# Kernel tuning notes

Measured on AMD Instinct MI355X. Metric: run time of the kernel, lower is better.

The kernel has to match this reference:

```python
import jax, jax.numpy as jnp
import numpy as np

CUBE_SIZE = 24
N_NEURONS = CUBE_SIZE ** 3  # 13824
INPUT_DIM = 512
OUTPUT_DIM = 1000
MAX_STEPS = 30
BATCH = 256


def _build_neighbor_indices(size: int) -> np.ndarray:
    """[N, 27] int32; invalid (out-of-cube) neighbors map to pad slot N."""
    n = size ** 3
    c = np.arange(size)
    z, y, x = np.meshgrid(c, c, c, indexing='ij')  # each [size,size,size]
    cols = []
    for dz in (-1, 0, 1):
        for dy in (-1, 0, 1):
            for dx in (-1, 0, 1):
                nz, ny, nx = z + dz, y + dy, x + dx
                valid = ((nz >= 0) & (nz < size) & (ny >= 0) & (ny < size)
                         & (nx >= 0) & (nx < size))
                idx = nz * size * size + ny * size + nx
                cols.append(np.where(valid, idx, n))
    return np.stack(cols, axis=-1).reshape(n, 27).astype(np.int32)


def setup_inputs() -> dict:
    key = jax.random.key(0)
    ks = jax.random.split(key, 4)
    # xavier-ish small init scales (gain 0.5 style)
    w_in = jax.random.normal(ks[0], (N_NEURONS, INPUT_DIM), jnp.float32) * 0.01
    w_local = jax.random.normal(ks[1], (N_NEURONS, 27), jnp.float32) * 0.1
    w_out = jax.random.normal(ks[2], (OUTPUT_DIM, N_NEURONS), jnp.float32) * 0.01
    x = jax.random.normal(ks[3], (BATCH, INPUT_DIM), jnp.float32)
    return {
        'x': x,
        'W_in_w': w_in,
        'W_in_b': jnp.zeros((N_NEURONS,), jnp.float32),
        'W_local': w_local,
        'W_out_w': w_out,
        'W_out_b': jnp.zeros((OUTPUT_DIM,), jnp.float32),
        'neighbor_indices': jnp.asarray(_build_neighbor_indices(CUBE_SIZE)),
    }


def reference(x, W_in_w, W_in_b, W_local, W_out_w, W_out_b, neighbor_indices):
    batch = x.shape[0]
    x_proj = x @ W_in_w.T + W_in_b  # [B, N]
    h0 = jnp.zeros((batch, N_NEURONS), x.dtype)
    pad = jnp.zeros((batch, 1), x.dtype)

    def step(h, _):
        h_padded = jnp.concatenate([h, pad], axis=1)        # [B, N+1]
        nbr = h_padded[:, neighbor_indices]                  # [B, N, 27]
        weighted = jnp.einsum('bnk,nk->bn', nbr, W_local)    # [B, N]
        return jnp.tanh(x_proj + weighted), None

    h, _ = jax.lax.scan(step, h0, None, length=MAX_STEPS)
    return h @ W_out_w.T + W_out_b  # [B, output_dim]
```

## Files before the change

kernel.cpp:

```cpp
#include <hip/hip_runtime.h>
#include <hip/hip_bf16.h>

#define NN   13824
#define BB   256
#define KDIM 512
#define ODIM 1000
#define CUBE 24
#define KS   16

typedef short bf8 __attribute__((ext_vector_type(8)));
typedef float f32x4 __attribute__((ext_vector_type(4)));

__device__ __forceinline__ float fast_tanh(float a) {
    float e = __expf(2.0f * a);
    return 1.0f - 2.0f / (e + 1.0f);
}
__device__ __forceinline__ float bf_lo(unsigned u) { return __uint_as_float(u << 16); }
__device__ __forceinline__ float bf_hi(unsigned u) { return __uint_as_float(u & 0xffff0000u); }
__device__ __forceinline__ unsigned short bf_rne(float f) {
    unsigned u = __float_as_uint(f);
    u += 0x7fffu + ((u >> 16) & 1u);
    return (unsigned short)(u >> 16);
}
__device__ __forceinline__ unsigned pk_bf16(float lo, float hi) {
    union { __hip_bfloat162 h; unsigned u; } cv;
    cv.h = __float22bfloat162_rn(make_float2(lo, hi));
    return cv.u;
}
__device__ __forceinline__ bf8 cvt8(float4 a, float4 b) {
    union { bf8 v; unsigned u[4]; } r;
    r.u[0] = pk_bf16(a.x, a.y);
    r.u[1] = pk_bf16(a.z, a.w);
    r.u[2] = pk_bf16(b.x, b.y);
    r.u[3] = pk_bf16(b.z, b.w);
    return r.v;
}

__global__ __launch_bounds__(256) void xbf_kernel(
    const float* __restrict__ x, unsigned* __restrict__ xb)
{
    int i = blockIdx.x * 256 + threadIdx.x;
    float2 v = *(const float2*)&x[(size_t)i * 2];
    xb[i] = pk_bf16(v.x, v.y);
}

__global__ __launch_bounds__(256) void xproj_mfma(
    const float* __restrict__ w_in, const float* __restrict__ bias,
    const short* __restrict__ xbf, unsigned short* __restrict__ xp,
    unsigned short* __restrict__ h1)
{
    const int tid = threadIdx.x, w = tid >> 6, lane = tid & 63;
    const int quad = lane >> 4, l16 = lane & 15;
    const int n0 = blockIdx.x * 16;
    const float* __restrict__ arow = &w_in[(size_t)(n0 + l16) * KDIM];

    f32x4 acc[4] = {};

    int ka = quad * 8;
    float4 a0 = *(const float4*)&arow[ka];
    float4 a1 = *(const float4*)&arow[ka + 4];
    bf8 bb[4];
#pragma unroll
    for (int j = 0; j < 4; ++j)
        bb[j] = *(const bf8*)&xbf[(size_t)(w * 64 + j * 16 + l16) * KDIM + ka];

    for (int it = 0; it < 16; ++it) {
        float4 na0{}, na1{}; bf8 nb[4] = {};
        if (it < 15) {
            const int nka = ka + 32;
            na0 = *(const float4*)&arow[nka];
            na1 = *(const float4*)&arow[nka + 4];
#pragma unroll
            for (int j = 0; j < 4; ++j)
                nb[j] = *(const bf8*)&xbf[(size_t)(w * 64 + j * 16 + l16) * KDIM + nka];
        }
        bf8 af = cvt8(a0, a1);
#pragma unroll
        for (int j = 0; j < 4; ++j)
            acc[j] = __builtin_amdgcn_mfma_f32_16x16x32_bf16(af, bb[j], acc[j], 0, 0, 0);
        a0 = na0; a1 = na1;
#pragma unroll
        for (int j = 0; j < 4; ++j) bb[j] = nb[j];
        ka += 32;
    }

#pragma unroll
    for (int j = 0; j < 4; ++j) {
        const int b = w * 64 + j * 16 + l16;
#pragma unroll
        for (int r = 0; r < 4; ++r) {
            const int n = n0 + quad * 4 + r;
            const float v = acc[j][r] + bias[n];
            xp[(size_t)n * BB + b] = bf_rne(v);
            h1[(size_t)n * BB + b] = bf_rne(fast_tanh(v));
        }
    }
}

__device__ __forceinline__ void load_plane_f2(
    const unsigned* __restrict__ h32, int z, int y, int xx, int dof, float2* w9)
{
#pragma unroll
    for (int j = 0; j < 9; ++j) {
        const int dz = j / 3 - 1, dy = j % 3 - 1;
        const int zz = z + dz, yy = y + dy;
        const bool valid = (xx >= 0) & (xx < CUBE) & (zz >= 0) & (zz < CUBE) &
                           (yy >= 0) & (yy < CUBE);
        unsigned v = 0u;
        if (valid) v = h32[(size_t)((zz * 24 + yy) * 24 + xx) * 128 + dof];
        w9[j] = make_float2(bf_lo(v), bf_hi(v));
    }
}

__global__ __launch_bounds__(256) void step_kernel(
    const unsigned* __restrict__ hprev, const unsigned* __restrict__ xp,
    const float* __restrict__ wl, unsigned* __restrict__ hnext)
{
    const int tid  = threadIdx.x;
    const int wid  = __builtin_amdgcn_readfirstlane(tid >> 6);
    const int wvb  = wid & 1;
    const int yoff = wid >> 1;
    const int lane = tid & 63;

    const int bid   = blockIdx.x;
    const int zhi   = bid & 7;
    const int inner = bid >> 3;
    const int yp    = inner % 12;
    const int r     = inner / 12;
    const int xc    = r & 3;
    const int zlo   = r >> 2;
    const int z     = zhi * 3 + zlo;
    const int y     = yp * 2 + yoff;

    const int x0   = xc * 6;
    const int dof  = wvb * 64 + lane;

    float2 win[5][9];
    load_plane_f2(hprev, z, y, x0 - 1, dof, win[0]);
    load_plane_f2(hprev, z, y, x0,     dof, win[1]);
    load_plane_f2(hprev, z, y, x0 + 1, dof, win[2]);
    load_plane_f2(hprev, z, y, x0 + 2, dof, win[3]);

#pragma unroll
    for (int xi = 0; xi < 6; ++xi) {
        const int x = x0 + xi;
        if (xi <= 3)
            load_plane_f2(hprev, z, y, x + 3, dof, win[(xi + 4) % 5]);

        const int n = (z * 24 + y) * 24 + x;
        const float* __restrict__ wn = &wl[(size_t)n * 27];
        const unsigned xpv = xp[(size_t)n * 128 + dof];
        float2 acc = make_float2(bf_lo(xpv), bf_hi(xpv));

        const float2* pm = win[xi % 5];
        const float2* pc = win[(xi + 1) % 5];
        const float2* pp = win[(xi + 2) % 5];
#pragma unroll
        for (int j = 0; j < 9; ++j) {
            const float w0 = wn[3 * j + 0];
            const float w1 = wn[3 * j + 1];
            const float w2 = wn[3 * j + 2];
            acc.x += w0 * pm[j].x + w1 * pc[j].x + w2 * pp[j].x;
            acc.y += w0 * pm[j].y + w1 * pc[j].y + w2 * pp[j].y;
        }
        hnext[(size_t)n * 128 + dof] = pk_bf16(fast_tanh(acc.x), fast_tanh(acc.y));
    }
}

__global__ __launch_bounds__(256) void transpose_kernel(
    const unsigned* __restrict__ h32, unsigned* __restrict__ hT32)
{
    __shared__ unsigned short T[64][66];
    const int tid = threadIdx.x;
    const int rr = tid >> 2, g = tid & 3;
    const int k0 = blockIdx.x * 64, b0 = blockIdx.y * 64;
#pragma unroll
    for (int i = 0; i < 8; ++i) {
        unsigned d = h32[(size_t)(k0 + rr) * 128 + b0 / 2 + g * 8 + i];
        const int bl = (g * 8 + i) * 2;
        T[bl][rr]     = (unsigned short)(d & 0xffffu);
        T[bl + 1][rr] = (unsigned short)(d >> 16);
    }
    __syncthreads();
#pragma unroll
    for (int i = 0; i < 8; ++i) {
        const int kl = (g * 8 + i) * 2;
        unsigned d = (unsigned)T[rr][kl] | ((unsigned)T[rr][kl + 1] << 16);
        hT32[(size_t)(b0 + rr) * (NN / 2) + k0 / 2 + g * 8 + i] = d;
    }
}

__global__ __launch_bounds__(256) void outgemm_mfma(
    const float* __restrict__ wout, const short* __restrict__ hT,
    float* __restrict__ part)
{
    const int tid = threadIdx.x, w = tid >> 6, lane = tid & 63;
    const int quad = lane >> 4, l16 = lane & 15;
    const int o0 = blockIdx.x * 128 + w * 32;
    const int kb = blockIdx.z * (NN / KS);
    const int b0 = blockIdx.y * 64;

    const int oa = o0 + l16, ob = o0 + 16 + l16;
    const bool av0 = oa < ODIM, av1 = ob < ODIM;
    const float* __restrict__ ar0 = &wout[(size_t)oa * NN];
    const float* __restrict__ ar1 = &wout[(size_t)ob * NN];
    const float4 z4 = {0.f, 0.f, 0.f, 0.f};

    f32x4 acc[2][4] = {};

    int ka = kb + quad * 8;
    float4 a00 = av0 ? *(const float4*)&ar0[ka]     : z4;
    float4 a01 = av0 ? *(const float4*)&ar0[ka + 4] : z4;
    float4 a10 = av1 ? *(const float4*)&ar1[ka]     : z4;
    float4 a11 = av1 ? *(const float4*)&ar1[ka + 4] : z4;
    bf8 bb[4];
#pragma unroll
    for (int j = 0; j < 4; ++j)
        bb[j] = *(const bf8*)&hT[(size_t)(b0 + j * 16 + l16) * NN + ka];

    for (int it = 0; it < 27; ++it) {
        float4 na00{}, na01{}, na10{}, na11{}; bf8 nb[4] = {};
        if (it < 26) {
            const int nka = ka + 32;
            na00 = av0 ? *(const float4*)&ar0[nka]     : z4;
            na01 = av0 ? *(const float4*)&ar0[nka + 4] : z4;
            na10 = av1 ? *(const float4*)&ar1[nka]     : z4;
            na11 = av1 ? *(const float4*)&ar1[nka + 4] : z4;
#pragma unroll
            for (int j = 0; j < 4; ++j)
                nb[j] = *(const bf8*)&hT[(size_t)(b0 + j * 16 + l16) * NN + nka];
        }
        bf8 af0 = cvt8(a00, a01);
        bf8 af1 = cvt8(a10, a11);
#pragma unroll
        for (int j = 0; j < 4; ++j) {
            acc[0][j] = __builtin_amdgcn_mfma_f32_16x16x32_bf16(af0, bb[j], acc[0][j], 0, 0, 0);
            acc[1][j] = __builtin_amdgcn_mfma_f32_16x16x32_bf16(af1, bb[j], acc[1][j], 0, 0, 0);
        }
        a00 = na00; a01 = na01; a10 = na10; a11 = na11;
#pragma unroll
        for (int j = 0; j < 4; ++j) bb[j] = nb[j];
        ka += 32;
    }

#pragma unroll
    for (int i = 0; i < 2; ++i)
#pragma unroll
        for (int j = 0; j < 4; ++j) {
            const int b = b0 + j * 16 + l16;
#pragma unroll
            for (int r = 0; r < 4; ++r) {
                const int o = o0 + i * 16 + quad * 4 + r;
                if (o < 1024)
                    part[((size_t)blockIdx.z * 1024 + o) * BB + b] = acc[i][j][r];
            }
        }
}

__global__ __launch_bounds__(256) void reduce_kernel(
    const float* __restrict__ part, const float* __restrict__ bias,
    float* __restrict__ out)
{
    const int o = blockIdx.x, b = threadIdx.x;
    float s = bias[o];
#pragma unroll
    for (int kc = 0; kc < KS; ++kc)
        s += part[((size_t)kc * 1024 + o) * BB + b];
    out[(size_t)b * ODIM + o] = s;
}

extern "C" void kernel_launch(void* const* d_in, const int* in_sizes, int n_in,
                              void* d_out, int out_size, void* d_ws, size_t ws_size,
                              hipStream_t stream)
{
    const float* x       = (const float*)d_in[0];
    const float* w_in    = (const float*)d_in[1];
    const float* b_in    = (const float*)d_in[2];
    const float* w_local = (const float*)d_in[3];
    const float* w_out   = (const float*)d_in[4];
    const float* b_out   = (const float*)d_in[5];
    float* out = (float*)d_out;

    char* p = (char*)d_ws;
    unsigned short* xp_bf = (unsigned short*)p;          p += (size_t)NN * BB * 2;
    unsigned short* hA    = (unsigned short*)p;          p += (size_t)NN * BB * 2;
    unsigned short* hB    = (unsigned short*)p;          p += (size_t)NN * BB * 2;
    unsigned short* hT    = (unsigned short*)p;          p += (size_t)NN * BB * 2;
    unsigned short* x_bf  = (unsigned short*)p;          p += (size_t)BB * KDIM * 2;
    float*          part  = (float*)p;

    xbf_kernel<<<256, 256, 0, stream>>>(x, (unsigned*)x_bf);
    xproj_mfma<<<864, 256, 0, stream>>>(w_in, b_in, (const short*)x_bf, xp_bf, hA);

    const unsigned* hp = (const unsigned*)hA;
    unsigned* hn = (unsigned*)hB;
    for (int s = 0; s < 29; ++s) {
        step_kernel<<<1152, 256, 0, stream>>>(hp, (const unsigned*)xp_bf, w_local, hn);
        unsigned* t = (unsigned*)hp; hp = hn; hn = t;
    }

    transpose_kernel<<<dim3(216, 4), 256, 0, stream>>>(hp, (unsigned*)hT);
    outgemm_mfma<<<dim3(8, 4, KS), 256, 0, stream>>>(w_out, (const short*)hT, part);
    reduce_kernel<<<ODIM, 256, 0, stream>>>(part, b_out, out);
}
```

Before: 559.2 us.

## Stage W_out tile in LDS as bf16 once per block, share across batch warps

Reorganizes the output GEMM so each block owns 32 output rows and a K-slice, loads that W_out slice once from global memory, converts it to bf16 and stores it in shared memory. The four warps then each cover 64 batch columns and read A fragments from LDS. Previously every warp streamed and converted its own fp32 W_out rows. The change removes redundant global W_out reads and conversions, at the cost of about 54KB of LDS per block and a new grid shape.

```diff
diff --git a/kernel.cpp b/kernel.cpp
--- a/kernel.cpp
+++ b/kernel.cpp
@@ -7,6 +7,7 @@
 #define ODIM 1000
 #define CUBE 24
 #define KS   16
+#define ASTR 872
 
 typedef short bf8 __attribute__((ext_vector_type(8)));
 typedef float f32x4 __attribute__((ext_vector_type(4)));
@@ -194,53 +195,61 @@
     const float* __restrict__ wout, const short* __restrict__ hT,
     float* __restrict__ part)
 {
+    __shared__ unsigned short As[32 * ASTR];
     const int tid = threadIdx.x, w = tid >> 6, lane = tid & 63;
     const int quad = lane >> 4, l16 = lane & 15;
-    const int o0 = blockIdx.x * 128 + w * 32;
-    const int kb = blockIdx.z * (NN / KS);
-    const int b0 = blockIdx.y * 64;
-
-    const int oa = o0 + l16, ob = o0 + 16 + l16;
-    const bool av0 = oa < ODIM, av1 = ob < ODIM;
-    const float* __restrict__ ar0 = &wout[(size_t)oa * NN];
-    const float* __restrict__ ar1 = &wout[(size_t)ob * NN];
-    const float4 z4 = {0.f, 0.f, 0.f, 0.f};
+    const int kb = blockIdx.x * (NN / KS);
+    const int o0 = blockIdx.y * 32;
+    const int b0 = w * 64;
+
+#pragma unroll
+    for (int rr = 0; rr < 8; ++rr) {
+        const int row = w * 8 + rr;
+        const int o = o0 + row;
+        const float* __restrict__ src = &wout[(size_t)o * NN + kb];
+#pragma unroll
+        for (int c = 0; c < 4; ++c) {
+            const int col = c * 256 + lane * 4;
+            if (c < 3 || lane < 24) {
+                float4 v = {0.f, 0.f, 0.f, 0.f};
+                if (o < ODIM) v = *(const float4*)&src[col];
+                uint2 pk2 = make_uint2(pk_bf16(v.x, v.y), pk_bf16(v.z, v.w));
+                *(uint2*)&As[(unsigned)row * ASTR + (unsigned)col] = pk2;
+            }
+        }
+    }
+    __syncthreads();
 
     f32x4 acc[2][4] = {};
 
-    int ka = kb + quad * 8;
-    float4 a00 = av0 ? *(const float4*)&ar0[ka]     : z4;
-    float4 a01 = av0 ? *(const float4*)&ar0[ka + 4] : z4;
-    float4 a10 = av1 ? *(const float4*)&ar1[ka]     : z4;
-    float4 a11 = av1 ? *(const float4*)&ar1[ka + 4] : z4;
     bf8 bb[4];
-#pragma unroll
-    for (int j = 0; j < 4; ++j)
-        bb[j] = *(const bf8*)&hT[(size_t)(b0 + j * 16 + l16) * NN + ka];
-
-    for (int it = 0; it < 27; ++it) {
-        float4 na00{}, na01{}, na10{}, na11{}; bf8 nb[4] = {};
-        if (it < 26) {
-            const int nka = ka + 32;
-            na00 = av0 ? *(const float4*)&ar0[nka]     : z4;
-            na01 = av0 ? *(const float4*)&ar0[nka + 4] : z4;
-            na10 = av1 ? *(const float4*)&ar1[nka]     : z4;
-            na11 = av1 ? *(const float4*)&ar1[nka + 4] : z4;
+    {
+        const int ka = kb + quad * 8;
+#pragma unroll
+        for (int j = 0; j < 4; ++j)
+            bb[j] = *(const bf8*)&hT[(size_t)(b0 + j * 16 + l16) * NN + ka];
+    }
+
+    const int r0 = l16, r1 = 16 + l16;
+
+    for (int kc = 0; kc < 27; ++kc) {
+        bf8 nb[4] = {};
+        if (kc < 26) {
+            const int ka = kb + (kc + 1) * 32 + quad * 8;
 #pragma unroll
             for (int j = 0; j < 4; ++j)
-                nb[j] = *(const bf8*)&hT[(size_t)(b0 + j * 16 + l16) * NN + nka];
-        }
-        bf8 af0 = cvt8(a00, a01);
-        bf8 af1 = cvt8(a10, a11);
+                nb[j] = *(const bf8*)&hT[(size_t)(b0 + j * 16 + l16) * NN + ka];
+        }
+        const int cs = kc * 32 + quad * 8;
+        bf8 a0 = *(const bf8*)&As[(unsigned)r0 * ASTR + (unsigned)cs];
+        bf8 a1 = *(const bf8*)&As[(unsigned)r1 * ASTR + (unsigned)cs];
 #pragma unroll
         for (int j = 0; j < 4; ++j) {
-            acc[0][j] = __builtin_amdgcn_mfma_f32_16x16x32_bf16(af0, bb[j], acc[0][j], 0, 0, 0);
-            acc[1][j] = __builtin_amdgcn_mfma_f32_16x16x32_bf16(af1, bb[j], acc[1][j], 0, 0, 0);
-        }
-        a00 = na00; a01 = na01; a10 = na10; a11 = na11;
+            acc[0][j] = __builtin_amdgcn_mfma_f32_16x16x32_bf16(a0, bb[j], acc[0][j], 0, 0, 0);
+            acc[1][j] = __builtin_amdgcn_mfma_f32_16x16x32_bf16(a1, bb[j], acc[1][j], 0, 0, 0);
+        }
 #pragma unroll
         for (int j = 0; j < 4; ++j) bb[j] = nb[j];
-        ka += 32;
     }
 
 #pragma unroll
@@ -251,8 +260,7 @@
 #pragma unroll
             for (int r = 0; r < 4; ++r) {
                 const int o = o0 + i * 16 + quad * 4 + r;
-                if (o < 1024)
-                    part[((size_t)blockIdx.z * 1024 + o) * BB + b] = acc[i][j][r];
+                part[((size_t)blockIdx.x * 1024 + o) * BB + b] = acc[i][j][r];
             }
         }
 }
@@ -300,6 +308,6 @@
     }
 
     transpose_kernel<<<dim3(216, 4), 256, 0, stream>>>(hp, (unsigned*)hT);
-    outgemm_mfma<<<dim3(8, 4, KS), 256, 0, stream>>>(w_out, (const short*)hT, part);
+    outgemm_mfma<<<dim3(KS, 32), 256, 0, stream>>>(w_out, (const short*)hT, part);
     reduce_kernel<<<ODIM, 256, 0, stream>>>(part, b_out, out);
 }
```

Result: no change. 552.9 us (-1.1%).
